# Kernel tuning notes

Measured on AMD Instinct MI355X. Metric: run time of the kernel, lower is better.

The kernel has to match this reference:

```python
import jax, jax.numpy as jnp
import numpy as np

EPS = 1e-5
P = 2  # polynomial kernel degree


def setup_inputs() -> dict:
    key = jax.random.key(0)
    k1, k2, k3 = jax.random.split(key, 3)
    b, t, h, d = 2, 2048, 8, 64
    Q = jax.random.normal(k1, (b, t, h, d), jnp.float32)
    K = jax.random.normal(k2, (b, t, h, d), jnp.float32)
    V = jax.random.normal(k3, (b, t, h, d), jnp.float32)
    return {"Q": Q, "K": K, "V": V, "chunk_count": 16}


def reference(Q, K, V, chunk_count):
    b, t, h, d = Q.shape
    dv = V.shape[-1]
    c = chunk_count
    n = t // c  # tokens per chunk

    def to_chunked(X):
        # [b, t, h, d] -> [c, b, h, n, d]
        return X.reshape(b, c, n, h, X.shape[-1]).transpose(1, 0, 3, 2, 4)

    Qc, Kc, Vc = to_chunked(Q), to_chunked(K), to_chunked(V)

    # ---- per-chunk states: s = K^T K, S = sum_n (K_n outer K_n) outer V_n ----
    s_loc = jnp.einsum('cbhni,cbhnj->cbhij', Kc, Kc)                 # [c,b,h,d,d]
    S_loc = jnp.einsum('cbhni,cbhnj,cbhnv->cbhijv', Kc, Kc, Vc)      # [c,b,h,d,d,dv]
    # inclusive cumulative merge over chunks
    S = jnp.cumsum(S_loc, axis=0)
    s = jnp.cumsum(s_loc, axis=0)

    # ---- local within-chunk masked quadratic attention ----
    D = jnp.einsum('cbhqi,cbhki->cbhqk', Qc, Kc)                     # [c,b,h,n,n]
    C = D ** P
    mask = jnp.tril(jnp.ones((n, n), dtype=bool))
    B = jnp.where(mask, C, 0.0)
    Y = jnp.einsum('cbhqk,cbhkv->cbhqv', B, Vc)                      # [c,b,h,n,dv]
    Z = B.sum(-1) + EPS                                              # [c,b,h,n]

    # ---- cross-chunk contribution: chunk i>0 attends to state of chunks <i ----
    Qp = Qc[1:]
    Sp, sp = S[:-1], s[:-1]
    num = jnp.einsum('cbhni,cbhnj,cbhijv->cbhnv', Qp, Qp, Sp)
    den = jnp.einsum('cbhni,cbhnj,cbhij->cbhn', Qp, Qp, sp)
    Y = Y.at[1:].add(num)
    Z = Z.at[1:].add(den)

    out = (Y / Z[..., None]).transpose(1, 0, 3, 2, 4).reshape(b, t, h, dv)
    return out
```

## Files before the change

### kernel.cpp

```cpp
#include <hip/hip_runtime.h>
#include <hip/hip_fp16.h>

typedef __attribute__((ext_vector_type(8))) _Float16 f16x8;
typedef __attribute__((ext_vector_type(4))) _Float16 f16x4;
typedef __attribute__((ext_vector_type(8))) unsigned short u16x8;
typedef __attribute__((ext_vector_type(4))) float f32x4;

constexpr int NT = 256;
constexpr int TILE_SHORTS = 4096;

__device__ __forceinline__ int swzoff(int row, int c) {
    return row * 64 + ((c ^ (row & 7)) << 3);
}
__device__ __forceinline__ unsigned short f2h_u(float x) {
    return __half_as_ushort(__float2half(x));
}

__global__ __launch_bounds__(256, 4) void prepass(
    const float* __restrict__ Kg, const float* __restrict__ Vg,
    unsigned short* __restrict__ Kw, unsigned short* __restrict__ Vw)
{
    __shared__ __align__(16) float Vl[64 * 68];
    const int tile = blockIdx.x;
    const int bh   = blockIdx.y;
    const int b = bh >> 3, h = bh & 7;
    const int tid = threadIdx.x;
    const size_t gbase = (((size_t)b * 2048 + tile * 64) * 8 + h) * 64;

    #pragma unroll
    for (int j = 0; j < 4; ++j) {
        int id = j * 256 + tid, row = id >> 4, c4 = id & 15;
        *(float4*)&Vl[row * 68 + c4 * 4] =
            *(const float4*)&Vg[gbase + (size_t)row * 512 + c4 * 4];
    }

    unsigned short* Ko = Kw + (size_t)(bh * 32 + tile) * TILE_SHORTS;
    #pragma unroll
    for (int j = 0; j < 2; ++j) {
        int id = j * 256 + tid, row = id >> 3, c = id & 7;
        const float* src = &Kg[gbase + (size_t)row * 512 + c * 8];
        float4 x = *(const float4*)src, y = *(const float4*)(src + 4);
        u16x8 o;
        o[0] = f2h_u(x.x); o[1] = f2h_u(x.y); o[2] = f2h_u(x.z); o[3] = f2h_u(x.w);
        o[4] = f2h_u(y.x); o[5] = f2h_u(y.y); o[6] = f2h_u(y.z); o[7] = f2h_u(y.w);
        *(u16x8*)&Ko[swzoff(row, c)] = o;
    }
    __syncthreads();

    unsigned short* Vo = Vw + (size_t)(bh * 32 + tile) * TILE_SHORTS;
    #pragma unroll
    for (int j = 0; j < 2; ++j) {
        int id = j * 256 + tid, vrow = id >> 3, g = id & 7;
        u16x8 o;
        #pragma unroll
        for (int jj = 0; jj < 8; ++jj) {
            int kk = ((g & 1) * 2 + (jj >> 2)) * 16 + (g >> 1) * 4 + (jj & 3);
            o[jj] = f2h_u(Vl[kk * 68 + vrow]);
        }
        *(u16x8*)&Vo[swzoff(vrow, g)] = o;
    }
}

__global__ __launch_bounds__(NT, 3) void attn_pow2_f16(
    const float* __restrict__ Qg,
    const unsigned short* __restrict__ Kw, const unsigned short* __restrict__ Vw,
    float* __restrict__ Og)
{
    __shared__ __align__(16) unsigned short lds[4 * TILE_SHORTS];
    unsigned short* const Kb = lds;
    unsigned short* const Vb = lds + 2 * TILE_SHORTS;
    const int tid  = threadIdx.x;
    const int lane = tid & 63;
    const int wave = tid >> 6;
    const int a    = lane & 15;
    const int quad = lane >> 4;
    const int m0   = wave * 16;

    int r0 = (int)blockIdx.x;
    int wr = (r0 < 256) ? r0 : (767 - r0);
    const int qt = 31 - (wr >> 4);
    const int bh = wr & 15;
    const int b = bh >> 3, h = bh & 7;
    const int q0 = qt * 64;

    f16x8 bQ[2];
    {
        const size_t qrowbase = (((size_t)b * 2048 + q0 + m0 + a) * 8 + h) * 64;
        #pragma unroll
        for (int ks = 0; ks < 2; ++ks) {
            const float* src = &Qg[qrowbase + ks * 32 + quad * 8];
            float4 x = *(const float4*)src, y = *(const float4*)(src + 4);
            u16x8 o;
            o[0] = f2h_u(x.x); o[1] = f2h_u(x.y); o[2] = f2h_u(x.z); o[3] = f2h_u(x.w);
            o[4] = f2h_u(y.x); o[5] = f2h_u(y.y); o[6] = f2h_u(y.z); o[7] = f2h_u(y.w);
            bQ[ks] = __builtin_bit_cast(f16x8, o);
        }
    }

    const unsigned short* Ktiles = Kw + (size_t)bh * 32 * TILE_SHORTS;
    const unsigned short* Vtiles = Vw + (size_t)bh * 32 * TILE_SHORTS;

    u16x8 rK[2], rV[2];
    auto gload = [&](int kt) {
        const u16x8* kg = (const u16x8*)(Ktiles + (size_t)kt * TILE_SHORTS);
        const u16x8* vg = (const u16x8*)(Vtiles + (size_t)kt * TILE_SHORTS);
        rK[0] = kg[tid * 2]; rK[1] = kg[tid * 2 + 1];
        rV[0] = vg[tid * 2]; rV[1] = vg[tid * 2 + 1];
    };
    gload(0);

    f32x4 oacc[4];
    #pragma unroll
    for (int n = 0; n < 4; ++n) oacc[n] = (f32x4){0.f, 0.f, 0.f, 0.f};
    float den_l = 0.f;

    union U8 { u16x8 u; f16x4 q[2]; f16x8 f; };

    for (int kt = 0; kt <= qt; ++kt) {
        const int buf = kt & 1;
        u16x8* kd = (u16x8*)(Kb + buf * TILE_SHORTS);
        u16x8* vd = (u16x8*)(Vb + buf * TILE_SHORTS);
        kd[tid * 2] = rK[0]; kd[tid * 2 + 1] = rK[1];
        vd[tid * 2] = rV[0]; vd[tid * 2 + 1] = rV[1];
        __syncthreads();
        if (kt < qt) gload(kt + 1);

        const unsigned short* Kc = Kb + buf * TILE_SHORTS;
        const unsigned short* Vc = Vb + buf * TILE_SHORTS;

        f32x4 sacc[4];
        #pragma unroll
        for (int s = 0; s < 4; ++s) sacc[s] = (f32x4){0.f, 0.f, 0.f, 0.f};
        #pragma unroll
        for (int s = 0; s < 4; ++s) {
            #pragma unroll
            for (int ks = 0; ks < 2; ++ks) {
                U8 ak; ak.u = *(const u16x8*)&Kc[swzoff(s * 16 + a, ks * 4 + quad)];
                sacc[s] = __builtin_amdgcn_mfma_f32_16x16x32_f16(ak.f, bQ[ks], sacc[s], 0, 0, 0);
            }
        }

        const bool diag = (kt == qt);
        f16x4 aS[4];
        #pragma unroll
        for (int s = 0; s < 4; ++s) {
            float p[4];
            #pragma unroll
            for (int r = 0; r < 4; ++r) {
                float d0 = sacc[s][r];
                float v = d0 * d0;
                if (diag && (s * 16 + quad * 4 + r) > (m0 + a)) v = 0.f;
                p[r] = v;
            }
            den_l += (p[0] + p[1]) + (p[2] + p[3]);
            aS[s] = (f16x4){(_Float16)p[0], (_Float16)p[1], (_Float16)p[2], (_Float16)p[3]};
        }

        #pragma unroll
        for (int n = 0; n < 4; ++n) {
            U8 va, vb;
            va.u = *(const u16x8*)&Vc[swzoff(n * 16 + a, quad * 2)];
            vb.u = *(const u16x8*)&Vc[swzoff(n * 16 + a, quad * 2 + 1)];
            oacc[n] = __builtin_amdgcn_mfma_f32_16x16x16f16(aS[0], va.q[0], oacc[n], 0, 0, 0);
            oacc[n] = __builtin_amdgcn_mfma_f32_16x16x16f16(aS[1], va.q[1], oacc[n], 0, 0, 0);
            oacc[n] = __builtin_amdgcn_mfma_f32_16x16x16f16(aS[2], vb.q[0], oacc[n], 0, 0, 0);
            oacc[n] = __builtin_amdgcn_mfma_f32_16x16x16f16(aS[3], vb.q[1], oacc[n], 0, 0, 0);
        }
    }

    den_l += __shfl_xor(den_l, 16);
    den_l += __shfl_xor(den_l, 32);

    float invz[4];
    #pragma unroll
    for (int r = 0; r < 4; ++r) {
        float dq = __shfl(den_l, quad * 4 + r);
        invz[r] = 1.0f / (dq + 1e-5f);
    }

    #pragma unroll
    for (int n = 0; n < 4; ++n) {
        #pragma unroll
        for (int r = 0; r < 4; ++r) {
            int t = q0 + m0 + quad * 4 + r;
            int v = n * 16 + a;
            Og[(((size_t)b * 2048 + t) * 8 + h) * 64 + v] = oacc[n][r] * invz[r];
        }
    }
}

extern "C" void kernel_launch(void* const* d_in, const int* in_sizes, int n_in,
                              void* d_out, int out_size, void* d_ws, size_t ws_size,
                              hipStream_t stream) {
    const float* Q = (const float*)d_in[0];
    const float* K = (const float*)d_in[1];
    const float* V = (const float*)d_in[2];
    float* O = (float*)d_out;
    unsigned short* Kw = (unsigned short*)d_ws;
    unsigned short* Vw = Kw + (size_t)16 * 32 * TILE_SHORTS;

    prepass<<<dim3(32, 16), 256, 0, stream>>>(K, V, Kw, Vw);
    attn_pow2_f16<<<dim3(512), NT, 0, stream>>>(Q, Kw, Vw, O);
}
```

Baseline: 95.20 us.

## Prefetch two K/V tiles ahead and remap blocks to XCDs by head

The attention loop now keeps two register sets and issues global loads two tiles ahead, alternating between the two LDS buffers, so memory latency gets more cover. Both kernels also remap the block index so that each XCD (bid&7) works on the same two (b,h) heads, which should improve L2 locality for the K/V tiles. The attention grid pairs a long and a short causal row on each head to balance load. The extra prefetch registers raise register pressure and may hurt occupancy at launch bounds of 3 waves per SIMD.

```diff
diff --git a/kernel.cpp b/kernel.cpp
--- a/kernel.cpp
+++ b/kernel.cpp
@@ -21,8 +21,11 @@
     unsigned short* __restrict__ Kw, unsigned short* __restrict__ Vw)
 {
     __shared__ __align__(16) float Vl[64 * 68];
-    const int tile = blockIdx.x;
-    const int bh   = blockIdx.y;
+    const int bid  = (int)blockIdx.x;
+    const int xcd  = bid & 7;
+    const int y    = bid >> 3;
+    const int bh   = xcd * 2 + (y >= 32);
+    const int tile = y & 31;
     const int b = bh >> 3, h = bh & 7;
     const int tid = threadIdx.x;
     const size_t gbase = (((size_t)b * 2048 + tile * 64) * 8 + h) * 64;
@@ -39,10 +42,10 @@
     for (int j = 0; j < 2; ++j) {
         int id = j * 256 + tid, row = id >> 3, c = id & 7;
         const float* src = &Kg[gbase + (size_t)row * 512 + c * 8];
-        float4 x = *(const float4*)src, y = *(const float4*)(src + 4);
+        float4 x = *(const float4*)src, y2 = *(const float4*)(src + 4);
         u16x8 o;
         o[0] = f2h_u(x.x); o[1] = f2h_u(x.y); o[2] = f2h_u(x.z); o[3] = f2h_u(x.w);
-        o[4] = f2h_u(y.x); o[5] = f2h_u(y.y); o[6] = f2h_u(y.z); o[7] = f2h_u(y.w);
+        o[4] = f2h_u(y2.x); o[5] = f2h_u(y2.y); o[6] = f2h_u(y2.z); o[7] = f2h_u(y2.w);
         *(u16x8*)&Ko[swzoff(row, c)] = o;
     }
     __syncthreads();
@@ -76,10 +79,12 @@
     const int quad = lane >> 4;
     const int m0   = wave * 16;
 
-    int r0 = (int)blockIdx.x;
-    int wr = (r0 < 256) ? r0 : (767 - r0);
-    const int qt = 31 - (wr >> 4);
-    const int bh = wr & 15;
+    const int bid = (int)blockIdx.x;
+    const int xcd = bid & 7;
+    const int y   = bid >> 3;
+    const int yy  = y & 31;
+    const int bh  = xcd * 2 + (y >= 32);
+    const int qt  = (y < 32) ? (31 - yy) : yy;
     const int b = bh >> 3, h = bh & 7;
     const int q0 = qt * 64;
 
@@ -89,10 +94,10 @@
         #pragma unroll
         for (int ks = 0; ks < 2; ++ks) {
             const float* src = &Qg[qrowbase + ks * 32 + quad * 8];
-            float4 x = *(const float4*)src, y = *(const float4*)(src + 4);
+            float4 x = *(const float4*)src, y2 = *(const float4*)(src + 4);
             u16x8 o;
             o[0] = f2h_u(x.x); o[1] = f2h_u(x.y); o[2] = f2h_u(x.z); o[3] = f2h_u(x.w);
-            o[4] = f2h_u(y.x); o[5] = f2h_u(y.y); o[6] = f2h_u(y.z); o[7] = f2h_u(y.w);
+            o[4] = f2h_u(y2.x); o[5] = f2h_u(y2.y); o[6] = f2h_u(y2.z); o[7] = f2h_u(y2.w);
             bQ[ks] = __builtin_bit_cast(f16x8, o);
         }
     }
@@ -100,14 +105,19 @@
     const unsigned short* Ktiles = Kw + (size_t)bh * 32 * TILE_SHORTS;
     const unsigned short* Vtiles = Vw + (size_t)bh * 32 * TILE_SHORTS;
 
-    u16x8 rK[2], rV[2];
-    auto gload = [&](int kt) {
+    u16x8 rKA[2], rVA[2], rKB[2], rVB[2];
+    auto gloadA = [&](int kt) {
         const u16x8* kg = (const u16x8*)(Ktiles + (size_t)kt * TILE_SHORTS);
         const u16x8* vg = (const u16x8*)(Vtiles + (size_t)kt * TILE_SHORTS);
-        rK[0] = kg[tid * 2]; rK[1] = kg[tid * 2 + 1];
-        rV[0] = vg[tid * 2]; rV[1] = vg[tid * 2 + 1];
+        rKA[0] = kg[tid * 2]; rKA[1] = kg[tid * 2 + 1];
+        rVA[0] = vg[tid * 2]; rVA[1] = vg[tid * 2 + 1];
     };
-    gload(0);
+    auto gloadB = [&](int kt) {
+        const u16x8* kg = (const u16x8*)(Ktiles + (size_t)kt * TILE_SHORTS);
+        const u16x8* vg = (const u16x8*)(Vtiles + (size_t)kt * TILE_SHORTS);
+        rKB[0] = kg[tid * 2]; rKB[1] = kg[tid * 2 + 1];
+        rVB[0] = vg[tid * 2]; rVB[1] = vg[tid * 2 + 1];
+    };
 
     f32x4 oacc[4];
     #pragma unroll
@@ -116,18 +126,8 @@
 
     union U8 { u16x8 u; f16x4 q[2]; f16x8 f; };
 
-    for (int kt = 0; kt <= qt; ++kt) {
-        const int buf = kt & 1;
-        u16x8* kd = (u16x8*)(Kb + buf * TILE_SHORTS);
-        u16x8* vd = (u16x8*)(Vb + buf * TILE_SHORTS);
-        kd[tid * 2] = rK[0]; kd[tid * 2 + 1] = rK[1];
-        vd[tid * 2] = rV[0]; vd[tid * 2 + 1] = rV[1];
-        __syncthreads();
-        if (kt < qt) gload(kt + 1);
-
-        const unsigned short* Kc = Kb + buf * TILE_SHORTS;
-        const unsigned short* Vc = Vb + buf * TILE_SHORTS;
-
+    auto compute = [&](const unsigned short* Kc, const unsigned short* Vc,
+                       bool diag) {
         f32x4 sacc[4];
         #pragma unroll
         for (int s = 0; s < 4; ++s) sacc[s] = (f32x4){0.f, 0.f, 0.f, 0.f};
@@ -140,7 +140,6 @@
             }
         }
 
-        const bool diag = (kt == qt);
         f16x4 aS[4];
         #pragma unroll
         for (int s = 0; s < 4; ++s) {
@@ -166,6 +165,34 @@
             oacc[n] = __builtin_amdgcn_mfma_f32_16x16x16f16(aS[2], vb.q[0], oacc[n], 0, 0, 0);
             oacc[n] = __builtin_amdgcn_mfma_f32_16x16x16f16(aS[3], vb.q[1], oacc[n], 0, 0, 0);
         }
+    };
+
+    gloadA(0);
+    if (qt >= 1) gloadB(1);
+
+    int kt = 0;
+    for (;;) {
+        {
+            u16x8* kd = (u16x8*)Kb;
+            u16x8* vd = (u16x8*)Vb;
+            kd[tid * 2] = rKA[0]; kd[tid * 2 + 1] = rKA[1];
+            vd[tid * 2] = rVA[0]; vd[tid * 2 + 1] = rVA[1];
+        }
+        __syncthreads();
+        if (kt + 2 <= qt) gloadA(kt + 2);
+        compute(Kb, Vb, kt == qt);
+        if (++kt > qt) break;
+
+        {
+            u16x8* kd = (u16x8*)(Kb + TILE_SHORTS);
+            u16x8* vd = (u16x8*)(Vb + TILE_SHORTS);
+            kd[tid * 2] = rKB[0]; kd[tid * 2 + 1] = rKB[1];
+            vd[tid * 2] = rVB[0]; vd[tid * 2 + 1] = rVB[1];
+        }
+        __syncthreads();
+        if (kt + 2 <= qt) gloadB(kt + 2);
+        compute(Kb + TILE_SHORTS, Vb + TILE_SHORTS, kt == qt);
+        if (++kt > qt) break;
     }
 
     den_l += __shfl_xor(den_l, 16);
@@ -199,6 +226,6 @@
     unsigned short* Kw = (unsigned short*)d_ws;
     unsigned short* Vw = Kw + (size_t)16 * 32 * TILE_SHORTS;
 
-    prepass<<<dim3(32, 16), 256, 0, stream>>>(K, V, Kw, Vw);
+    prepass<<<dim3(512), 256, 0, stream>>>(K, V, Kw, Vw);
     attn_pow2_f16<<<dim3(512), NT, 0, stream>>>(Q, Kw, Vw, O);
 }
```

Result: slower. 99.76 us (+4.8%).

## Fuse K/V fp16 prepass into attention kernel via cooperative grid sync

Applied to the files above, without the earlier changes.

Merges the separate K/V fp16 conversion prepass into the attention kernel. Each block converts one K/V tile, then a cooperative grid-wide barrier ensures all tiles are written before the attention loop starts, removing one kernel launch and the gap between launches. Block-to-work mapping is also changed so each XCD handles two batch-heads, pairing causal-heavy and causal-light query tiles. The cost is a grid sync, a stricter occupancy requirement (launch bounds lowered to 2 blocks per CU), and the cooperative launch overhead.

```diff
diff --git a/kernel.cpp b/kernel.cpp
--- a/kernel.cpp
+++ b/kernel.cpp
@@ -1,5 +1,8 @@
 #include <hip/hip_runtime.h>
 #include <hip/hip_fp16.h>
+#include <hip/hip_cooperative_groups.h>
+
+namespace cg = cooperative_groups;
 
 typedef __attribute__((ext_vector_type(8))) _Float16 f16x8;
 typedef __attribute__((ext_vector_type(4))) _Float16 f16x4;
@@ -16,59 +19,13 @@
     return __half_as_ushort(__float2half(x));
 }
 
-__global__ __launch_bounds__(256, 4) void prepass(
+__global__ __launch_bounds__(NT, 2) void fused_attn(
+    const float* __restrict__ Qg,
     const float* __restrict__ Kg, const float* __restrict__ Vg,
-    unsigned short* __restrict__ Kw, unsigned short* __restrict__ Vw)
-{
-    __shared__ __align__(16) float Vl[64 * 68];
-    const int tile = blockIdx.x;
-    const int bh   = blockIdx.y;
-    const int b = bh >> 3, h = bh & 7;
-    const int tid = threadIdx.x;
-    const size_t gbase = (((size_t)b * 2048 + tile * 64) * 8 + h) * 64;
-
-    #pragma unroll
-    for (int j = 0; j < 4; ++j) {
-        int id = j * 256 + tid, row = id >> 4, c4 = id & 15;
-        *(float4*)&Vl[row * 68 + c4 * 4] =
-            *(const float4*)&Vg[gbase + (size_t)row * 512 + c4 * 4];
-    }
-
-    unsigned short* Ko = Kw + (size_t)(bh * 32 + tile) * TILE_SHORTS;
-    #pragma unroll
-    for (int j = 0; j < 2; ++j) {
-        int id = j * 256 + tid, row = id >> 3, c = id & 7;
-        const float* src = &Kg[gbase + (size_t)row * 512 + c * 8];
-        float4 x = *(const float4*)src, y = *(const float4*)(src + 4);
-        u16x8 o;
-        o[0] = f2h_u(x.x); o[1] = f2h_u(x.y); o[2] = f2h_u(x.z); o[3] = f2h_u(x.w);
-        o[4] = f2h_u(y.x); o[5] = f2h_u(y.y); o[6] = f2h_u(y.z); o[7] = f2h_u(y.w);
-        *(u16x8*)&Ko[swzoff(row, c)] = o;
-    }
-    __syncthreads();
-
-    unsigned short* Vo = Vw + (size_t)(bh * 32 + tile) * TILE_SHORTS;
-    #pragma unroll
-    for (int j = 0; j < 2; ++j) {
-        int id = j * 256 + tid, vrow = id >> 3, g = id & 7;
-        u16x8 o;
-        #pragma unroll
-        for (int jj = 0; jj < 8; ++jj) {
-            int kk = ((g & 1) * 2 + (jj >> 2)) * 16 + (g >> 1) * 4 + (jj & 3);
-            o[jj] = f2h_u(Vl[kk * 68 + vrow]);
-        }
-        *(u16x8*)&Vo[swzoff(vrow, g)] = o;
-    }
-}
-
-__global__ __launch_bounds__(NT, 3) void attn_pow2_f16(
-    const float* __restrict__ Qg,
-    const unsigned short* __restrict__ Kw, const unsigned short* __restrict__ Vw,
+    unsigned short* __restrict__ Kw, unsigned short* __restrict__ Vw,
     float* __restrict__ Og)
 {
     __shared__ __align__(16) unsigned short lds[4 * TILE_SHORTS];
-    unsigned short* const Kb = lds;
-    unsigned short* const Vb = lds + 2 * TILE_SHORTS;
     const int tid  = threadIdx.x;
     const int lane = tid & 63;
     const int wave = tid >> 6;
@@ -76,10 +33,12 @@
     const int quad = lane >> 4;
     const int m0   = wave * 16;
 
-    int r0 = (int)blockIdx.x;
-    int wr = (r0 < 256) ? r0 : (767 - r0);
-    const int qt = 31 - (wr >> 4);
-    const int bh = wr & 15;
+    const int bid = (int)blockIdx.x;
+    const int xcd = bid & 7;
+    const int y   = bid >> 3;
+    const int yy  = y & 31;
+    const int bh  = xcd * 2 + (y >= 32);
+    const int qt  = (y < 32) ? (31 - yy) : yy;
     const int b = bh >> 3, h = bh & 7;
     const int q0 = qt * 64;
 
@@ -89,13 +48,57 @@
         #pragma unroll
         for (int ks = 0; ks < 2; ++ks) {
             const float* src = &Qg[qrowbase + ks * 32 + quad * 8];
-            float4 x = *(const float4*)src, y = *(const float4*)(src + 4);
+            float4 x = *(const float4*)src, y2 = *(const float4*)(src + 4);
             u16x8 o;
             o[0] = f2h_u(x.x); o[1] = f2h_u(x.y); o[2] = f2h_u(x.z); o[3] = f2h_u(x.w);
-            o[4] = f2h_u(y.x); o[5] = f2h_u(y.y); o[6] = f2h_u(y.z); o[7] = f2h_u(y.w);
+            o[4] = f2h_u(y2.x); o[5] = f2h_u(y2.y); o[6] = f2h_u(y2.z); o[7] = f2h_u(y2.w);
             bQ[ks] = __builtin_bit_cast(f16x8, o);
         }
     }
+
+    {
+        float* Vl = (float*)lds;
+        const int tile = qt;
+        const size_t gbase = (((size_t)b * 2048 + tile * 64) * 8 + h) * 64;
+
+        #pragma unroll
+        for (int j = 0; j < 4; ++j) {
+            int id = j * 256 + tid, row = id >> 4, c4 = id & 15;
+            *(float4*)&Vl[row * 68 + c4 * 4] =
+                *(const float4*)&Vg[gbase + (size_t)row * 512 + c4 * 4];
+        }
+
+        unsigned short* Ko = Kw + (size_t)(bh * 32 + tile) * TILE_SHORTS;
+        #pragma unroll
+        for (int j = 0; j < 2; ++j) {
+            int id = j * 256 + tid, row = id >> 3, c = id & 7;
+            const float* src = &Kg[gbase + (size_t)row * 512 + c * 8];
+            float4 x = *(const float4*)src, y2 = *(const float4*)(src + 4);
+            u16x8 o;
+            o[0] = f2h_u(x.x); o[1] = f2h_u(x.y); o[2] = f2h_u(x.z); o[3] = f2h_u(x.w);
+            o[4] = f2h_u(y2.x); o[5] = f2h_u(y2.y); o[6] = f2h_u(y2.z); o[7] = f2h_u(y2.w);
+            *(u16x8*)&Ko[swzoff(row, c)] = o;
+        }
+        __syncthreads();
+
+        unsigned short* Vo = Vw + (size_t)(bh * 32 + tile) * TILE_SHORTS;
+        #pragma unroll
+        for (int j = 0; j < 2; ++j) {
+            int id = j * 256 + tid, vrow = id >> 3, g = id & 7;
+            u16x8 o;
+            #pragma unroll
+            for (int jj = 0; jj < 8; ++jj) {
+                int kk = ((g & 1) * 2 + (jj >> 2)) * 16 + (g >> 1) * 4 + (jj & 3);
+                o[jj] = f2h_u(Vl[kk * 68 + vrow]);
+            }
+            *(u16x8*)&Vo[swzoff(vrow, g)] = o;
+        }
+    }
+
+    cg::this_grid().sync();
+
+    unsigned short* const Kb = lds;
+    unsigned short* const Vb = lds + 2 * TILE_SHORTS;
 
     const unsigned short* Ktiles = Kw + (size_t)bh * 32 * TILE_SHORTS;
     const unsigned short* Vtiles = Vw + (size_t)bh * 32 * TILE_SHORTS;
@@ -199,6 +202,8 @@
     unsigned short* Kw = (unsigned short*)d_ws;
     unsigned short* Vw = Kw + (size_t)16 * 32 * TILE_SHORTS;
 
-    prepass<<<dim3(32, 16), 256, 0, stream>>>(K, V, Kw, Vw);
-    attn_pow2_f16<<<dim3(512), NT, 0, stream>>>(Q, Kw, Vw, O);
-}
+    void* args[] = {(void*)&Q, (void*)&K, (void*)&V,
+                    (void*)&Kw, (void*)&Vw, (void*)&O};
+    hipLaunchCooperativeKernel((const void*)fused_attn,
+                               dim3(512), dim3(NT), args, 0, stream);
+}
```

Result: slower. 158.4 us (+66.3%).

## Split key tiles across wave pairs with 32-row query blocks and LDS reduction

Applied to the files above, without the earlier changes.

Each wave now handles 32 query rows instead of 16, so every K fragment loaded from LDS feeds two MFMAs. The two wave pairs take alternating key tiles (even/odd) and merge partial outputs and denominators through LDS at the end. This halves per-wave LDS fragment traffic per MFMA but roughly doubles accumulator registers, so the launch-bounds occupancy hint drops from 3 to 2. Half the waves sit idle at each tile, and a final cross-wave reduction is added.

```diff
diff --git a/kernel.cpp b/kernel.cpp
--- a/kernel.cpp
+++ b/kernel.cpp
@@ -61,7 +61,7 @@
     }
 }
 
-__global__ __launch_bounds__(NT, 3) void attn_pow2_f16(
+__global__ __launch_bounds__(NT, 2) void attn_pow2_f16(
     const float* __restrict__ Qg,
     const unsigned short* __restrict__ Kw, const unsigned short* __restrict__ Vw,
     float* __restrict__ Og)
@@ -69,12 +69,13 @@
     __shared__ __align__(16) unsigned short lds[4 * TILE_SHORTS];
     unsigned short* const Kb = lds;
     unsigned short* const Vb = lds + 2 * TILE_SHORTS;
-    const int tid  = threadIdx.x;
-    const int lane = tid & 63;
-    const int wave = tid >> 6;
-    const int a    = lane & 15;
-    const int quad = lane >> 4;
-    const int m0   = wave * 16;
+    const int tid   = threadIdx.x;
+    const int lane  = tid & 63;
+    const int wave  = tid >> 6;
+    const int a     = lane & 15;
+    const int quad  = lane >> 4;
+    const int qhalf = wave & 1;
+    const int par   = wave >> 1;
 
     int r0 = (int)blockIdx.x;
     int wr = (r0 < 256) ? r0 : (767 - r0);
@@ -83,9 +84,11 @@
     const int b = bh >> 3, h = bh & 7;
     const int q0 = qt * 64;
 
-    f16x8 bQ[2];
-    {
-        const size_t qrowbase = (((size_t)b * 2048 + q0 + m0 + a) * 8 + h) * 64;
+    f16x8 bQ[2][2];
+    #pragma unroll
+    for (int mi = 0; mi < 2; ++mi) {
+        const int mb = qhalf * 32 + mi * 16;
+        const size_t qrowbase = (((size_t)b * 2048 + q0 + mb + a) * 8 + h) * 64;
         #pragma unroll
         for (int ks = 0; ks < 2; ++ks) {
             const float* src = &Qg[qrowbase + ks * 32 + quad * 8];
@@ -93,7 +96,7 @@
             u16x8 o;
             o[0] = f2h_u(x.x); o[1] = f2h_u(x.y); o[2] = f2h_u(x.z); o[3] = f2h_u(x.w);
             o[4] = f2h_u(y.x); o[5] = f2h_u(y.y); o[6] = f2h_u(y.z); o[7] = f2h_u(y.w);
-            bQ[ks] = __builtin_bit_cast(f16x8, o);
+            bQ[mi][ks] = __builtin_bit_cast(f16x8, o);
         }
     }
 
@@ -109,10 +112,12 @@
     };
     gload(0);
 
-    f32x4 oacc[4];
-    #pragma unroll
-    for (int n = 0; n < 4; ++n) oacc[n] = (f32x4){0.f, 0.f, 0.f, 0.f};
-    float den_l = 0.f;
+    f32x4 oacc[2][4];
+    #pragma unroll
+    for (int mi = 0; mi < 2; ++mi)
+        #pragma unroll
+        for (int n = 0; n < 4; ++n) oacc[mi][n] = (f32x4){0.f, 0.f, 0.f, 0.f};
+    float den_l[2] = {0.f, 0.f};
 
     union U8 { u16x8 u; f16x4 q[2]; f16x8 f; };
 
@@ -125,66 +130,108 @@
         __syncthreads();
         if (kt < qt) gload(kt + 1);
 
-        const unsigned short* Kc = Kb + buf * TILE_SHORTS;
-        const unsigned short* Vc = Vb + buf * TILE_SHORTS;
-
-        f32x4 sacc[4];
-        #pragma unroll
-        for (int s = 0; s < 4; ++s) sacc[s] = (f32x4){0.f, 0.f, 0.f, 0.f};
-        #pragma unroll
-        for (int s = 0; s < 4; ++s) {
-            #pragma unroll
-            for (int ks = 0; ks < 2; ++ks) {
-                U8 ak; ak.u = *(const u16x8*)&Kc[swzoff(s * 16 + a, ks * 4 + quad)];
-                sacc[s] = __builtin_amdgcn_mfma_f32_16x16x32_f16(ak.f, bQ[ks], sacc[s], 0, 0, 0);
-            }
-        }
-
-        const bool diag = (kt == qt);
-        f16x4 aS[4];
-        #pragma unroll
-        for (int s = 0; s < 4; ++s) {
-            float p[4];
+        if ((kt & 1) == par) {
+            const unsigned short* Kc = Kb + buf * TILE_SHORTS;
+            const unsigned short* Vc = Vb + buf * TILE_SHORTS;
+            const bool diag = (kt == qt);
+
+            f32x4 sacc[2][4];
+            #pragma unroll
+            for (int mi = 0; mi < 2; ++mi)
+                #pragma unroll
+                for (int s = 0; s < 4; ++s) sacc[mi][s] = (f32x4){0.f, 0.f, 0.f, 0.f};
+            #pragma unroll
+            for (int s = 0; s < 4; ++s) {
+                #pragma unroll
+                for (int ks = 0; ks < 2; ++ks) {
+                    U8 ak; ak.u = *(const u16x8*)&Kc[swzoff(s * 16 + a, ks * 4 + quad)];
+                    sacc[0][s] = __builtin_amdgcn_mfma_f32_16x16x32_f16(ak.f, bQ[0][ks], sacc[0][s], 0, 0, 0);
+                    sacc[1][s] = __builtin_amdgcn_mfma_f32_16x16x32_f16(ak.f, bQ[1][ks], sacc[1][s], 0, 0, 0);
+                }
+            }
+
+            f16x4 aS[2][4];
+            #pragma unroll
+            for (int mi = 0; mi < 2; ++mi) {
+                const int mb = qhalf * 32 + mi * 16;
+                #pragma unroll
+                for (int s = 0; s < 4; ++s) {
+                    float p[4];
+                    #pragma unroll
+                    for (int r = 0; r < 4; ++r) {
+                        float d0 = sacc[mi][s][r];
+                        float v = d0 * d0;
+                        if (diag && (s * 16 + quad * 4 + r) > (mb + a)) v = 0.f;
+                        p[r] = v;
+                    }
+                    den_l[mi] += (p[0] + p[1]) + (p[2] + p[3]);
+                    aS[mi][s] = (f16x4){(_Float16)p[0], (_Float16)p[1],
+                                        (_Float16)p[2], (_Float16)p[3]};
+                }
+            }
+
+            #pragma unroll
+            for (int n = 0; n < 4; ++n) {
+                U8 va, vb;
+                va.u = *(const u16x8*)&Vc[swzoff(n * 16 + a, quad * 2)];
+                vb.u = *(const u16x8*)&Vc[swzoff(n * 16 + a, quad * 2 + 1)];
+                #pragma unroll
+                for (int mi = 0; mi < 2; ++mi) {
+                    oacc[mi][n] = __builtin_amdgcn_mfma_f32_16x16x16f16(aS[mi][0], va.q[0], oacc[mi][n], 0, 0, 0);
+                    oacc[mi][n] = __builtin_amdgcn_mfma_f32_16x16x16f16(aS[mi][1], va.q[1], oacc[mi][n], 0, 0, 0);
+                    oacc[mi][n] = __builtin_amdgcn_mfma_f32_16x16x16f16(aS[mi][2], vb.q[0], oacc[mi][n], 0, 0, 0);
+                    oacc[mi][n] = __builtin_amdgcn_mfma_f32_16x16x16f16(aS[mi][3], vb.q[1], oacc[mi][n], 0, 0, 0);
+                }
+            }
+        }
+    }
+
+    __syncthreads();
+    f32x4* xo = (f32x4*)lds;
+    float*  xd = (float*)((char*)lds + 16384);
+    if (par == 1) {
+        #pragma unroll
+        for (int n = 0; n < 4; ++n)
+            #pragma unroll
+            for (int mi = 0; mi < 2; ++mi)
+                xo[(((n * 2 + mi) * 2) + qhalf) * 64 + lane] = oacc[mi][n];
+        xd[(qhalf * 2 + 0) * 64 + lane] = den_l[0];
+        xd[(qhalf * 2 + 1) * 64 + lane] = den_l[1];
+    }
+    __syncthreads();
+    if (par == 0) {
+        #pragma unroll
+        for (int n = 0; n < 4; ++n)
+            #pragma unroll
+            for (int mi = 0; mi < 2; ++mi)
+                oacc[mi][n] += xo[(((n * 2 + mi) * 2) + qhalf) * 64 + lane];
+        den_l[0] += xd[(qhalf * 2 + 0) * 64 + lane];
+        den_l[1] += xd[(qhalf * 2 + 1) * 64 + lane];
+
+        #pragma unroll
+        for (int mi = 0; mi < 2; ++mi) {
+            den_l[mi] += __shfl_xor(den_l[mi], 16);
+            den_l[mi] += __shfl_xor(den_l[mi], 32);
+        }
+
+        #pragma unroll
+        for (int mi = 0; mi < 2; ++mi) {
+            float invz[4];
             #pragma unroll
             for (int r = 0; r < 4; ++r) {
-                float d0 = sacc[s][r];
-                float v = d0 * d0;
-                if (diag && (s * 16 + quad * 4 + r) > (m0 + a)) v = 0.f;
-                p[r] = v;
-            }
-            den_l += (p[0] + p[1]) + (p[2] + p[3]);
-            aS[s] = (f16x4){(_Float16)p[0], (_Float16)p[1], (_Float16)p[2], (_Float16)p[3]};
-        }
-
-        #pragma unroll
-        for (int n = 0; n < 4; ++n) {
-            U8 va, vb;
-            va.u = *(const u16x8*)&Vc[swzoff(n * 16 + a, quad * 2)];
-            vb.u = *(const u16x8*)&Vc[swzoff(n * 16 + a, quad * 2 + 1)];
-            oacc[n] = __builtin_amdgcn_mfma_f32_16x16x16f16(aS[0], va.q[0], oacc[n], 0, 0, 0);
-            oacc[n] = __builtin_amdgcn_mfma_f32_16x16x16f16(aS[1], va.q[1], oacc[n], 0, 0, 0);
-            oacc[n] = __builtin_amdgcn_mfma_f32_16x16x16f16(aS[2], vb.q[0], oacc[n], 0, 0, 0);
-            oacc[n] = __builtin_amdgcn_mfma_f32_16x16x16f16(aS[3], vb.q[1], oacc[n], 0, 0, 0);
-        }
-    }
-
-    den_l += __shfl_xor(den_l, 16);
-    den_l += __shfl_xor(den_l, 32);
-
-    float invz[4];
-    #pragma unroll
-    for (int r = 0; r < 4; ++r) {
-        float dq = __shfl(den_l, quad * 4 + r);
-        invz[r] = 1.0f / (dq + 1e-5f);
-    }
-
-    #pragma unroll
-    for (int n = 0; n < 4; ++n) {
-        #pragma unroll
-        for (int r = 0; r < 4; ++r) {
-            int t = q0 + m0 + quad * 4 + r;
-            int v = n * 16 + a;
-            Og[(((size_t)b * 2048 + t) * 8 + h) * 64 + v] = oacc[n][r] * invz[r];
+                float dq = __shfl(den_l[mi], quad * 4 + r);
+                invz[r] = 1.0f / (dq + 1e-5f);
+            }
+            const int mb = qhalf * 32 + mi * 16;
+            #pragma unroll
+            for (int n = 0; n < 4; ++n) {
+                #pragma unroll
+                for (int r = 0; r < 4; ++r) {
+                    int t = q0 + mb + quad * 4 + r;
+                    int v = n * 16 + a;
+                    Og[(((size_t)b * 2048 + t) * 8 + h) * 64 + v] = oacc[mi][n][r] * invz[r];
+                }
+            }
         }
     }
 }
```

Result: slower. 108.5 us (+14.0%).
